# Kernel tuning notes

Hardware: AMD Instinct MI355X
Metric: run time of the kernel (lower is better)

The kernel has to match this reference:

```python
import jax, jax.numpy as jnp
import numpy as np

N = 100_000      # nodes
E = 1_600_000    # edges
F_IN = 64        # num_node_features
F = 64           # features_size
OUT = 1          # output_size
V = 2            # variants
A = 6            # activities per variant (second_encoder applied after each)
P = 8192         # (place, src, dst) triples per activity step


def setup_inputs() -> dict:
    key = jax.random.key(0)
    ks = jax.random.split(key, 16)
    s = 1.0 / np.sqrt(F)
    return {
        "x": jax.random.normal(ks[0], (N, F_IN), jnp.float32),
        "edge_index": jax.random.randint(ks[1], (2, E), 0, N, dtype=jnp.int32),
        "places": jax.random.randint(ks[2], (V, A, P), 0, N, dtype=jnp.int32),
        "srcs": jax.random.randint(ks[3], (V, A, P), 0, N, dtype=jnp.int32),
        "dsts": jax.random.randint(ks[4], (V, A, P), 0, N, dtype=jnp.int32),
        "W1": jax.random.normal(ks[5], (F_IN, F), jnp.float32) * s,
        "Wself1": jax.random.normal(ks[6], (F_IN, F), jnp.float32) * s,
        "b1": jnp.zeros((F,), jnp.float32),
        "W2": jax.random.normal(ks[7], (F, F), jnp.float32) * s,
        "Wself2": jax.random.normal(ks[8], (F, F), jnp.float32) * s,
        "b2": jnp.zeros((F,), jnp.float32),
        "Wd1": jax.random.normal(ks[9], (3 * F, F), jnp.float32) * s,
        "bd1": jnp.zeros((F,), jnp.float32),
        "Wd2": jax.random.normal(ks[10], (F, OUT), jnp.float32) * s,
        "bd2": jnp.zeros((OUT,), jnp.float32),
    }


def _gcn(h, edge_src, edge_dst, W, Wself, b):
    # message passing: sum-aggregate neighbor features, then linear + relu
    agg = jax.ops.segment_sum(h[edge_src], edge_dst, num_segments=N)  # [N, F]
    return jax.nn.relu(agg @ W + h @ Wself + b)


def reference(x, edge_index, places, srcs, dsts,
              W1, Wself1, b1, W2, Wself2, b2, Wd1, bd1, Wd2, bd2):
    edge_src, edge_dst = edge_index[0], edge_index[1]

    def decode(feat, p, s, d):
        # gather-concat-MLP-logsigmoid per (place, src, dst) triple
        cat = jnp.concatenate([feat[p], feat[s], feat[d]], axis=-1)  # [P, 3F]
        h = jax.nn.relu(cat @ Wd1 + bd1)
        return jax.nn.log_sigmoid(h @ Wd2 + bd2)                     # [P, OUT]

    feat0 = _gcn(x, edge_src, edge_dst, W1, Wself1, b1)  # first_encoder
    predictions = jnp.zeros((N, OUT), x.dtype)
    for v in range(V):
        feat = feat0  # features reset to post-first-encoder per variant
        pred = jnp.zeros((N, OUT), x.dtype)
        prev_prob = jnp.zeros((OUT,), x.dtype)
        for a in range(A):
            p, s, d = places[v, a], srcs[v, a], dsts[v, a]
            pp = decode(feat, p, s, d)          # [P, OUT]
            pred = pred.at[p].add(pp)           # scatter per place
            prev_prob = prev_prob + pred[p].sum(axis=0)
            pred = pred.at[p].add(prev_prob)    # broadcast to predicted places
            feat = _gcn(feat, edge_src, edge_dst, W2, Wself2, b2)  # second_encoder
        predictions = predictions + pred
    return predictions
```

## Files before the change

kernel.cpp:

```cpp
#include <hip/hip_runtime.h>
#include <hip/hip_bf16.h>

#define F 64
#define VARIANTS 2
#define ACTS 6


__global__ void k_hist(const int* __restrict__ dst, int* __restrict__ deg, int e) {
    int i = blockIdx.x * blockDim.x + threadIdx.x;
    if (i < e) atomicAdd(&deg[dst[i]], 1);
}

__global__ void k_scan1(const int* __restrict__ deg, int* __restrict__ rs,
                        int* __restrict__ bsum, int n) {
    __shared__ int sh[256];
    const int tid = threadIdx.x;
    const int base = blockIdx.x * 1024 + tid * 4;
    int v0 = (base + 0 < n) ? deg[base + 0] : 0;
    int v1 = (base + 1 < n) ? deg[base + 1] : 0;
    int v2 = (base + 2 < n) ? deg[base + 2] : 0;
    int v3 = (base + 3 < n) ? deg[base + 3] : 0;
    const int tsum = v0 + v1 + v2 + v3;
    sh[tid] = tsum;
    __syncthreads();
    for (int off = 1; off < 256; off <<= 1) {
        int t = (tid >= off) ? sh[tid - off] : 0;
        __syncthreads();
        sh[tid] += t;
        __syncthreads();
    }
    int excl = sh[tid] - tsum;
    if (base + 0 < n) rs[base + 0] = excl; excl += v0;
    if (base + 1 < n) rs[base + 1] = excl; excl += v1;
    if (base + 2 < n) rs[base + 2] = excl; excl += v2;
    if (base + 3 < n) rs[base + 3] = excl;
    if (tid == 255) bsum[blockIdx.x] = sh[255];
}

__global__ void k_scan2(int* __restrict__ bsum, int nb) {
    __shared__ int sh[128];
    const int tid = threadIdx.x;
    int v = (tid < nb) ? bsum[tid] : 0;
    sh[tid] = v;
    __syncthreads();
    for (int off = 1; off < 128; off <<= 1) {
        int t = (tid >= off) ? sh[tid - off] : 0;
        __syncthreads();
        sh[tid] += t;
        __syncthreads();
    }
    if (tid < nb) bsum[tid] = sh[tid] - v;
}

__global__ void k_scan3(int* __restrict__ rs, const int* __restrict__ bsum,
                        int* __restrict__ cursor, int n, int total) {
    const int base = blockIdx.x * 1024 + threadIdx.x * 4;
    const int off = bsum[blockIdx.x];
    #pragma unroll
    for (int j = 0; j < 4; ++j) {
        int i = base + j;
        if (i < n) {
            int v = rs[i] + off;
            rs[i] = v;
            cursor[i] = v;
        }
    }
    if (blockIdx.x == 0 && threadIdx.x == 0) rs[n] = total;
}

__global__ void k_fill(const int* __restrict__ src, const int* __restrict__ dst,
                       int* __restrict__ cursor, int* __restrict__ csr, int e) {
    int i = blockIdx.x * blockDim.x + threadIdx.x;
    if (i < e) {
        int pos = atomicAdd(&cursor[dst[i]], 1);
        csr[pos] = src[i];
    }
}

__global__ __launch_bounds__(256) void k_agg(
    const float* __restrict__ hin, const int* __restrict__ rs,
    const int* __restrict__ csr, float* __restrict__ agg, int n)
{
    const int tid = threadIdx.x;
    const int lane = tid & 63;
    const int nd = blockIdx.x * 4 + (tid >> 6);
    if (nd >= n) return;
    const int beg = rs[nd], end = rs[nd + 1];
    const int sub = lane >> 4;
    const int f4  = lane & 15;
    float ax = 0.f, ay = 0.f, az = 0.f, aw = 0.f;
    for (int cb = beg + sub; cb < end; cb += 4) {
        const int s = csr[cb];
        const float4 v = ((const float4*)(hin + (size_t)s * F))[f4];
        ax += v.x; ay += v.y; az += v.z; aw += v.w;
    }
    #pragma unroll
    for (int o = 16; o <= 32; o <<= 1) {
        ax += __shfl_xor(ax, o);
        ay += __shfl_xor(ay, o);
        az += __shfl_xor(az, o);
        aw += __shfl_xor(aw, o);
    }
    if (sub == 0) {
        float4 r; r.x = ax; r.y = ay; r.z = az; r.w = aw;
        ((float4*)(agg + (size_t)nd * F))[f4] = r;
    }
}

__global__ __launch_bounds__(256) void k_linear(
    const float* __restrict__ agg, const float* __restrict__ hin,
    const float* __restrict__ W, const float* __restrict__ Wself,
    const float* __restrict__ bias, float* __restrict__ out, int n)
{
    const int lane = threadIdx.x & 63;
    const int wv = blockIdx.x * 4 + (threadIdx.x >> 6);
    float wc[64], wsc[64];
    #pragma unroll
    for (int k = 0; k < 64; ++k) {
        wc[k]  = W[k * F + lane];
        wsc[k] = Wself[k * F + lane];
    }
    const float bf = bias[lane];
    const int base = wv * 8;
    #pragma unroll
    for (int t = 0; t < 8; ++t) {
        const int nd = base + t;
        if (nd < n) {
            const float4* __restrict__ ar4 = (const float4*)(agg + (size_t)nd * F);
            const float4* __restrict__ hr4 = (const float4*)(hin + (size_t)nd * F);
            float a = bf;
            #pragma unroll
            for (int q = 0; q < 16; ++q) {
                const float4 v = ar4[q];
                a = fmaf(v.x, wc[q * 4 + 0], a);
                a = fmaf(v.y, wc[q * 4 + 1], a);
                a = fmaf(v.z, wc[q * 4 + 2], a);
                a = fmaf(v.w, wc[q * 4 + 3], a);
            }
            #pragma unroll
            for (int q = 0; q < 16; ++q) {
                const float4 v = hr4[q];
                a = fmaf(v.x, wsc[q * 4 + 0], a);
                a = fmaf(v.y, wsc[q * 4 + 1], a);
                a = fmaf(v.z, wsc[q * 4 + 2], a);
                a = fmaf(v.w, wsc[q * 4 + 3], a);
            }
            out[(size_t)nd * F + lane] = fmaxf(a, 0.f);
        }
    }
}

__global__ __launch_bounds__(256) void k_decode2(
    const float* __restrict__ feat,
    const int* __restrict__ places, const int* __restrict__ srcs, const int* __restrict__ dsts,
    int a, const float* __restrict__ Wd1, const float* __restrict__ bd1,
    const float* __restrict__ Wd2, const float* __restrict__ bd2,
    float* __restrict__ pp, int nT, int bpv)
{
    const int v   = blockIdx.x / bpv;
    const int blk = blockIdx.x % bpv;
    const size_t ofs = ((size_t)v * ACTS + a) * nT;
    const int* __restrict__ pi = places + ofs;
    const int* __restrict__ si = srcs   + ofs;
    const int* __restrict__ di = dsts   + ofs;
    float* __restrict__ ppv = pp + (size_t)v * nT;

    const int lane = threadIdx.x & 63;
    const int wv = blk * 4 + (threadIdx.x >> 6);
    const int base = wv * 8;
    if (base >= nT) return;
    float acc[8];
    const float b0 = bd1[lane];
    #pragma unroll
    for (int t = 0; t < 8; ++t) acc[t] = b0;

    #pragma unroll
    for (int g = 0; g < 3; ++g) {
        const int* __restrict__ idx = (g == 0) ? pi : (g == 1) ? si : di;
        const float* __restrict__ Wg = Wd1 + (size_t)g * 64 * F;
        float wc[64];
        #pragma unroll
        for (int k = 0; k < 64; ++k) wc[k] = Wg[k * F + lane];
        #pragma unroll
        for (int t = 0; t < 8; ++t) {
            const int tri = base + t;
            if (tri < nT) {
                const int nd = idx[tri];
                const float4* __restrict__ row4 = (const float4*)(feat + (size_t)nd * F);
                float a2 = acc[t];
                #pragma unroll
                for (int q = 0; q < 16; ++q) {
                    const float4 vv = row4[q];
                    a2 = fmaf(vv.x, wc[q * 4 + 0], a2);
                    a2 = fmaf(vv.y, wc[q * 4 + 1], a2);
                    a2 = fmaf(vv.z, wc[q * 4 + 2], a2);
                    a2 = fmaf(vv.w, wc[q * 4 + 3], a2);
                }
                acc[t] = a2;
            }
        }
    }
    const float w2 = Wd2[lane];
    const float b2v = bd2[0];
    #pragma unroll
    for (int t = 0; t < 8; ++t) {
        const int tri = base + t;
        if (tri < nT) {
            float h = fmaxf(acc[t], 0.f);
            float vv = h * w2;
            #pragma unroll
            for (int o = 32; o; o >>= 1) vv += __shfl_xor(vv, o);
            if (lane == 0) {
                float z = vv + b2v;
                ppv[tri] = fminf(z, 0.f) - log1pf(expf(-fabsf(z)));
            }
        }
    }
}

__global__ __launch_bounds__(1024) void k_scatter2(
    const float* __restrict__ pp, const int* __restrict__ places, int a,
    float* __restrict__ pred01, float* __restrict__ prev01, int nP, int strideN)
{
    const int v = blockIdx.x;
    const int* __restrict__ p = places + ((size_t)v * ACTS + a) * nP;
    const float* __restrict__ ppv = pp + (size_t)v * nP;
    float* __restrict__ pred = pred01 + (size_t)v * strideN;
    float* __restrict__ prev = prev01 + v;

    __shared__ float wsum[16];
    __shared__ float s_tot;
    const int tid = threadIdx.x;
    for (int i = tid; i < nP; i += 1024) atomicAdd(&pred[p[i]], ppv[i]);
    __threadfence();
    __syncthreads();
    float s = 0.f;
    for (int i = tid; i < nP; i += 1024)
        s += __hip_atomic_load(&pred[p[i]], __ATOMIC_RELAXED, __HIP_MEMORY_SCOPE_AGENT);
    #pragma unroll
    for (int o = 32; o; o >>= 1) s += __shfl_down(s, o);
    if ((tid & 63) == 0) wsum[tid >> 6] = s;
    __syncthreads();
    if (tid == 0) {
        float tot = 0.f;
        #pragma unroll
        for (int w = 0; w < 16; ++w) tot += wsum[w];
        tot += *prev;
        *prev = tot;
        s_tot = tot;
    }
    __syncthreads();
    const float tot = s_tot;
    __threadfence();
    for (int i = tid; i < nP; i += 1024) atomicAdd(&pred[p[i]], tot);
}

__global__ void k_sum2(const float* __restrict__ pred01, float* __restrict__ out,
                       int n, int strideN) {
    int i = blockIdx.x * blockDim.x + threadIdx.x;
    if (i < n) out[i] = pred01[i] + pred01[(size_t)strideN + i];
}


extern "C" void kernel_launch(void* const* d_in, const int* in_sizes, int n_in,
                              void* d_out, int out_size, void* d_ws, size_t ws_size,
                              hipStream_t stream) {
    const float* x      = (const float*)d_in[0];
    const int*   eidx   = (const int*)d_in[1];
    const int*   places = (const int*)d_in[2];
    const int*   srcs   = (const int*)d_in[3];
    const int*   dsts   = (const int*)d_in[4];
    const float* W1     = (const float*)d_in[5];
    const float* Wself1 = (const float*)d_in[6];
    const float* b1     = (const float*)d_in[7];
    const float* W2     = (const float*)d_in[8];
    const float* Wself2 = (const float*)d_in[9];
    const float* b2     = (const float*)d_in[10];
    const float* Wd1    = (const float*)d_in[11];
    const float* bd1    = (const float*)d_in[12];
    const float* Wd2    = (const float*)d_in[13];
    const float* bd2    = (const float*)d_in[14];
    float* out          = (float*)d_out;

    const int N = in_sizes[0] / F;
    const int E = in_sizes[1] / 2;
    const int P = in_sizes[2] / (VARIANTS * ACTS);

    const int* edge_src = eidx;
    const int* edge_dst = eidx + E;

    size_t off = 0;
    auto carve = [&](size_t bytes) -> void* {
        void* ptr = (char*)d_ws + off;
        off += (bytes + 255) & ~(size_t)255;
        return ptr;
    };
    int*   deg    = (int*)carve((size_t)N * 4);
    int*   rs     = (int*)carve((size_t)(N + 1) * 4);
    int*   cursor = (int*)carve((size_t)N * 4);
    int*   csr    = (int*)carve((size_t)E * 4);
    int*   bsum   = (int*)carve(128 * 4);
    float* feat0  = (float*)carve((size_t)N * F * 4);
    float* featB  = (float*)carve((size_t)N * F * 4);
    float* featC  = (float*)carve((size_t)N * F * 4);
    float* agg    = (float*)carve((size_t)N * F * 4);
    float* pp2    = (float*)carve((size_t)VARIANTS * P * 4);
    float* pred01 = (float*)carve((size_t)VARIANTS * N * 4);
    float* prev01 = (float*)carve(256);
    (void)ws_size;

    const int nbScan   = (N + 1023) / 1024;
    const int blkE     = (E + 255) / 256;
    const int blkAgg   = (N + 3) / 4;
    const int blkLin   = (N + 31) / 32;
    const int bpv      = (P + 31) / 32;
    const int blkAdd   = (N + 255) / 256;

    (void)hipMemsetAsync(deg, 0, (size_t)N * 4, stream);
    (void)hipMemsetAsync(pred01, 0, (size_t)VARIANTS * N * 4, stream);
    (void)hipMemsetAsync(prev01, 0, 8, stream);

    k_hist <<<blkE, 256, 0, stream>>>(edge_dst, deg, E);
    k_scan1<<<nbScan, 256, 0, stream>>>(deg, rs, bsum, N);
    k_scan2<<<1, 128, 0, stream>>>(bsum, nbScan);
    k_scan3<<<nbScan, 256, 0, stream>>>(rs, bsum, cursor, N, E);
    k_fill <<<blkE, 256, 0, stream>>>(edge_src, edge_dst, cursor, csr, E);

    k_agg   <<<blkAgg, 256, 0, stream>>>(x, rs, csr, agg, N);
    k_linear<<<blkLin, 256, 0, stream>>>(agg, x, W1, Wself1, b1, feat0, N);

    const float* cur = feat0;
    for (int a = 0; a < ACTS; ++a) {
        k_decode2<<<2 * bpv, 256, 0, stream>>>(cur, places, srcs, dsts, a,
                                               Wd1, bd1, Wd2, bd2, pp2, P, bpv);
        k_scatter2<<<2, 1024, 0, stream>>>(pp2, places, a, pred01, prev01, P, N);
        if (a < ACTS - 1) {
            float* nxt = (cur == featB) ? featC : featB;
            k_agg   <<<blkAgg, 256, 0, stream>>>(cur, rs, csr, agg, N);
            k_linear<<<blkLin, 256, 0, stream>>>(agg, cur, W2, Wself2, b2, nxt, N);
            cur = nxt;
        }
    }
    k_sum2<<<blkAdd, 256, 0, stream>>>(pred01, out, N, N);
}
```

Baseline: 1.860 ms.

## Defer per-activity scatters into one final kernel and merge workspace memsets

Decode outputs for all activities are now kept in a per-(variant, activity) buffer, and the six tiny 2-block scatter launches are replaced by one kernel that runs the sequential scatter and prefix-sum loop for every activity at the end. The running prev-prob total moves into shared memory. This takes the small serial scatter kernels off the critical path between the decode and GCN launches. The two memsets are merged into one by placing deg and pred01 next to each other in the workspace, and k_fill is split into two half-range launches, which adds a launch and has no clear benefit.

Result: no change. 1.852 ms (-0.4%).

```diff
diff --git a/kernel.cpp b/kernel.cpp
--- a/kernel.cpp
+++ b/kernel.cpp
@@ -69,9 +69,9 @@
 }
 
 __global__ void k_fill(const int* __restrict__ src, const int* __restrict__ dst,
-                       int* __restrict__ cursor, int* __restrict__ csr, int e) {
-    int i = blockIdx.x * blockDim.x + threadIdx.x;
-    if (i < e) {
+                       int* __restrict__ cursor, int* __restrict__ csr, int e0, int e1) {
+    int i = e0 + blockIdx.x * blockDim.x + threadIdx.x;
+    if (i < e1) {
         int pos = atomicAdd(&cursor[dst[i]], 1);
         csr[pos] = src[i];
     }
@@ -155,7 +155,7 @@
     const int* __restrict__ places, const int* __restrict__ srcs, const int* __restrict__ dsts,
     int a, const float* __restrict__ Wd1, const float* __restrict__ bd1,
     const float* __restrict__ Wd2, const float* __restrict__ bd2,
-    float* __restrict__ pp, int nT, int bpv)
+    float* __restrict__ pp_all, int nT, int bpv)
 {
     const int v   = blockIdx.x / bpv;
     const int blk = blockIdx.x % bpv;
@@ -163,7 +163,7 @@
     const int* __restrict__ pi = places + ofs;
     const int* __restrict__ si = srcs   + ofs;
     const int* __restrict__ di = dsts   + ofs;
-    float* __restrict__ ppv = pp + (size_t)v * nT;
+    float* __restrict__ ppv = pp_all + ofs;
 
     const int lane = threadIdx.x & 63;
     const int wv = blk * 4 + (threadIdx.x >> 6);
@@ -218,41 +218,48 @@
     }
 }
 
-__global__ __launch_bounds__(1024) void k_scatter2(
-    const float* __restrict__ pp, const int* __restrict__ places, int a,
-    float* __restrict__ pred01, float* __restrict__ prev01, int nP, int strideN)
+__global__ __launch_bounds__(1024) void k_scatter_all(
+    const float* __restrict__ pp_all, const int* __restrict__ places,
+    float* __restrict__ pred01, int nP, int strideN)
 {
     const int v = blockIdx.x;
-    const int* __restrict__ p = places + ((size_t)v * ACTS + a) * nP;
-    const float* __restrict__ ppv = pp + (size_t)v * nP;
     float* __restrict__ pred = pred01 + (size_t)v * strideN;
-    float* __restrict__ prev = prev01 + v;
-
     __shared__ float wsum[16];
     __shared__ float s_tot;
+    __shared__ float s_prev;
     const int tid = threadIdx.x;
-    for (int i = tid; i < nP; i += 1024) atomicAdd(&pred[p[i]], ppv[i]);
-    __threadfence();
+    if (tid == 0) s_prev = 0.f;
     __syncthreads();
-    float s = 0.f;
-    for (int i = tid; i < nP; i += 1024)
-        s += __hip_atomic_load(&pred[p[i]], __ATOMIC_RELAXED, __HIP_MEMORY_SCOPE_AGENT);
-    #pragma unroll
-    for (int o = 32; o; o >>= 1) s += __shfl_down(s, o);
-    if ((tid & 63) == 0) wsum[tid >> 6] = s;
-    __syncthreads();
-    if (tid == 0) {
-        float tot = 0.f;
+
+    for (int a = 0; a < ACTS; ++a) {
+        const size_t ofs = ((size_t)v * ACTS + a) * nP;
+        const int* __restrict__ p = places + ofs;
+        const float* __restrict__ ppv = pp_all + ofs;
+        for (int i = tid; i < nP; i += 1024) atomicAdd(&pred[p[i]], ppv[i]);
+        __threadfence();
+        __syncthreads();
+        float s = 0.f;
+        for (int i = tid; i < nP; i += 1024)
+            s += __hip_atomic_load(&pred[p[i]], __ATOMIC_RELAXED, __HIP_MEMORY_SCOPE_AGENT);
         #pragma unroll
-        for (int w = 0; w < 16; ++w) tot += wsum[w];
-        tot += *prev;
-        *prev = tot;
-        s_tot = tot;
-    }
-    __syncthreads();
-    const float tot = s_tot;
-    __threadfence();
-    for (int i = tid; i < nP; i += 1024) atomicAdd(&pred[p[i]], tot);
+        for (int o = 32; o; o >>= 1) s += __shfl_down(s, o);
+        if ((tid & 63) == 0) wsum[tid >> 6] = s;
+        __syncthreads();
+        if (tid == 0) {
+            float tot = 0.f;
+            #pragma unroll
+            for (int w = 0; w < 16; ++w) tot += wsum[w];
+            tot += s_prev;
+            s_prev = tot;
+            s_tot = tot;
+        }
+        __syncthreads();
+        const float tot = s_tot;
+        __threadfence();
+        for (int i = tid; i < nP; i += 1024) atomicAdd(&pred[p[i]], tot);
+        __threadfence();
+        __syncthreads();
+    }
 }
 
 __global__ void k_sum2(const float* __restrict__ pred01, float* __restrict__ out,
@@ -296,6 +303,8 @@
         return ptr;
     };
     int*   deg    = (int*)carve((size_t)N * 4);
+    float* pred01 = (float*)carve((size_t)VARIANTS * N * 4);
+    const size_t zbytes = off;
     int*   rs     = (int*)carve((size_t)(N + 1) * 4);
     int*   cursor = (int*)carve((size_t)N * 4);
     int*   csr    = (int*)carve((size_t)E * 4);
@@ -304,27 +313,26 @@
     float* featB  = (float*)carve((size_t)N * F * 4);
     float* featC  = (float*)carve((size_t)N * F * 4);
     float* agg    = (float*)carve((size_t)N * F * 4);
-    float* pp2    = (float*)carve((size_t)VARIANTS * P * 4);
-    float* pred01 = (float*)carve((size_t)VARIANTS * N * 4);
-    float* prev01 = (float*)carve(256);
+    float* pp_all = (float*)carve((size_t)VARIANTS * ACTS * P * 4);
     (void)ws_size;
 
     const int nbScan   = (N + 1023) / 1024;
-    const int blkE     = (E + 255) / 256;
+    const int Ehalf    = E / 2;
+    const int blkEh    = (Ehalf + 255) / 256;
+    const int blkE2    = (E - Ehalf + 255) / 256;
     const int blkAgg   = (N + 3) / 4;
     const int blkLin   = (N + 31) / 32;
     const int bpv      = (P + 31) / 32;
     const int blkAdd   = (N + 255) / 256;
 
-    (void)hipMemsetAsync(deg, 0, (size_t)N * 4, stream);
-    (void)hipMemsetAsync(pred01, 0, (size_t)VARIANTS * N * 4, stream);
-    (void)hipMemsetAsync(prev01, 0, 8, stream);
-
-    k_hist <<<blkE, 256, 0, stream>>>(edge_dst, deg, E);
+    (void)hipMemsetAsync(d_ws, 0, zbytes, stream);
+
+    k_hist <<<(E + 255) / 256, 256, 0, stream>>>(edge_dst, deg, E);
     k_scan1<<<nbScan, 256, 0, stream>>>(deg, rs, bsum, N);
     k_scan2<<<1, 128, 0, stream>>>(bsum, nbScan);
     k_scan3<<<nbScan, 256, 0, stream>>>(rs, bsum, cursor, N, E);
-    k_fill <<<blkE, 256, 0, stream>>>(edge_src, edge_dst, cursor, csr, E);
+    k_fill <<<blkEh, 256, 0, stream>>>(edge_src, edge_dst, cursor, csr, 0, Ehalf);
+    k_fill <<<blkE2, 256, 0, stream>>>(edge_src, edge_dst, cursor, csr, Ehalf, E);
 
     k_agg   <<<blkAgg, 256, 0, stream>>>(x, rs, csr, agg, N);
     k_linear<<<blkLin, 256, 0, stream>>>(agg, x, W1, Wself1, b1, feat0, N);
@@ -332,8 +340,7 @@
     const float* cur = feat0;
     for (int a = 0; a < ACTS; ++a) {
         k_decode2<<<2 * bpv, 256, 0, stream>>>(cur, places, srcs, dsts, a,
-                                               Wd1, bd1, Wd2, bd2, pp2, P, bpv);
-        k_scatter2<<<2, 1024, 0, stream>>>(pp2, places, a, pred01, prev01, P, N);
+                                               Wd1, bd1, Wd2, bd2, pp_all, P, bpv);
         if (a < ACTS - 1) {
             float* nxt = (cur == featB) ? featC : featB;
             k_agg   <<<blkAgg, 256, 0, stream>>>(cur, rs, csr, agg, N);
@@ -341,5 +348,6 @@
             cur = nxt;
         }
     }
+    k_scatter_all<<<VARIANTS, 1024, 0, stream>>>(pp_all, places, pred01, P, N);
     k_sum2<<<blkAdd, 256, 0, stream>>>(pred01, out, N, N);
 }
```
